# Kernel optimization log

Hardware: AMD Instinct MI355X
Metric: run time of the kernel (lower is better)

## Reference

```python
import jax, jax.numpy as jnp
import numpy as np

D_MODEL, D_INNER, D_STATE, D_CONV, DT_RANK = 2048, 4096, 16, 4, 128
B, T = 2, 1024


def setup_inputs() -> dict:
    key = jax.random.key(0)
    ks = jax.random.split(key, 8)
    dt_init_std = DT_RANK ** -0.5
    # dt bias init per the torch code: inv softplus of dt in [dt_min, dt_max]
    dt = jnp.exp(jax.random.uniform(ks[6], (D_INNER,)) * (np.log(0.1) - np.log(0.001)) + np.log(0.001))
    dt = jnp.clip(dt, 1e-4, None)
    dt_proj_b = dt + jnp.log(-jnp.expm1(-dt))
    A_log = jnp.log(jnp.tile(jnp.arange(1, D_STATE + 1, dtype=jnp.float32)[None, :], (D_INNER, 1)))
    return {
        "x": jax.random.normal(ks[0], (B, T, D_MODEL), jnp.float32),
        "h": jnp.zeros((B, D_INNER, D_STATE), jnp.float32),
        "conv_cache": jnp.zeros((B, D_INNER, D_CONV - 1), jnp.float32),
        "in_proj_w": jax.random.normal(ks[1], (2 * D_INNER, D_MODEL), jnp.float32) * 0.02,
        "conv_w": jax.random.normal(ks[2], (D_INNER, D_CONV), jnp.float32) * (1.0 / np.sqrt(D_CONV)),
        "conv_b": jnp.zeros((D_INNER,), jnp.float32),
        "x_proj_w": jax.random.normal(ks[3], (DT_RANK + 2 * D_STATE, D_INNER), jnp.float32) * 0.02,
        "dt_proj_w": jax.random.uniform(ks[4], (D_INNER, DT_RANK), jnp.float32, -dt_init_std, dt_init_std),
        "dt_proj_b": dt_proj_b,
        "A_log": A_log,
        "D_param": jnp.ones((D_INNER,), jnp.float32),
        "out_proj_w": jax.random.normal(ks[5], (D_MODEL, D_INNER), jnp.float32) * 0.02,
    }


def _forward(x, h, conv_cache, in_proj_w, conv_w, conv_b, x_proj_w,
             dt_proj_w, dt_proj_b, A_log, D_param, out_proj_w):
    Tlen = x.shape[1]
    xz = x @ in_proj_w.T                                  # (B,T,2*d_inner)
    xi, z = jnp.split(xz, 2, axis=-1)
    # causal depthwise conv with cache: concat history then valid conv
    xc = jnp.concatenate([jnp.swapaxes(conv_cache, 1, 2), xi], axis=1)  # (B,T+3,d_inner)
    new_conv_cache = jnp.swapaxes(xc[:, -(D_CONV - 1):, :], 1, 2)       # (B,d_inner,3)
    xconv = sum(xc[:, k:k + Tlen, :] * conv_w[:, k] for k in range(D_CONV)) + conv_b
    xs = jax.nn.silu(xconv)                               # (B,T,d_inner)
    # SSM params per step
    dbc = xs @ x_proj_w.T                                 # (B,T,dt_rank+2n)
    delta, Bm, Cm = jnp.split(dbc, [DT_RANK, DT_RANK + D_STATE], axis=-1)
    delta = jax.nn.softplus(delta @ dt_proj_w.T + dt_proj_b)  # (B,T,d_inner)
    A = -jnp.exp(A_log)                                   # (d_inner,n)
    dA = jnp.exp(jnp.einsum('btd,dn->btdn', delta, A))    # (B,T,d,n)
    dBx = jnp.einsum('btd,btn,btd->btdn', delta, Bm, xs)  # (B,T,d,n)

    def step(hc, inp):
        dA_t, dBx_t, C_t = inp
        hc = dA_t * hc + dBx_t                            # (B,d,n)
        return hc, jnp.einsum('bdn,bn->bd', hc, C_t)

    h_last, ys = jax.lax.scan(
        step, h,
        (jnp.moveaxis(dA, 1, 0), jnp.moveaxis(dBx, 1, 0), jnp.moveaxis(Cm, 1, 0)))
    y = jnp.moveaxis(ys, 0, 1) + D_param * xs             # (B,T,d_inner)
    out = (y * jax.nn.silu(z)) @ out_proj_w.T             # (B,T,d_model)
    return out, h_last, new_conv_cache


def reference(x, h, conv_cache, in_proj_w, conv_w, conv_b, x_proj_w,
              dt_proj_w, dt_proj_b, A_log, D_param, out_proj_w):
    return _forward(x, h, conv_cache, in_proj_w, conv_w, conv_b, x_proj_w,
                    dt_proj_w, dt_proj_b, A_log, D_param, out_proj_w)
```

## Files before the change

kernel.cpp:

```cpp
#include <hip/hip_runtime.h>
#include <hip/hip_bf16.h>
#include <math.h>

#define D_MODEL 2048
#define D_INNER 4096
#define D_STATE 16
#define D_CONV  4
#define DT_RANK 128
#define NB      2
#define TT      1024
#define M_TOT   (NB * TT)
#define NC      16
#define CL      64
#define TC      16

typedef __bf16 bf16x8_t __attribute__((ext_vector_type(8)));
typedef __bf16 bf16x4_t __attribute__((ext_vector_type(4)));
typedef float  f32x4_t  __attribute__((ext_vector_type(4)));

__global__ __launch_bounds__(256) void fused_cast(
    const float* __restrict__ x,  const float* __restrict__ wi,
    const float* __restrict__ wo, const float* __restrict__ wx,
    const float* __restrict__ wdt,
    __bf16* __restrict__ x16,  __bf16* __restrict__ wi16,
    __bf16* __restrict__ wo16, __bf16* __restrict__ wx16,
    __bf16* __restrict__ wdt16, __bf16* __restrict__ dbc16)
{
    const size_t g = (size_t)blockIdx.x * 256 + threadIdx.x;
    const float* src; __bf16* dst; size_t off;
    if      (g < 524288)  { src = x;   dst = x16;   off = g; }
    else if (g < 2621440) { src = wi;  dst = wi16;  off = g - 524288; }
    else if (g < 3670016) { src = wo;  dst = wo16;  off = g - 2621440; }
    else if (g < 3801088) { off = g - 3670016; dst = wx16;
                            src = (g < 3751936) ? wx : nullptr; }
    else if (g < 3866624) { src = wdt; dst = wdt16; off = g - 3801088; }
    else                  { src = nullptr; dst = dbc16; off = g - 3866624; }

    bf16x8_t v;
    if (src) {
        const float4 f0 = ((const float4*)src)[2 * off];
        const float4 f1 = ((const float4*)src)[2 * off + 1];
        v[0] = (__bf16)f0.x; v[1] = (__bf16)f0.y; v[2] = (__bf16)f0.z; v[3] = (__bf16)f0.w;
        v[4] = (__bf16)f1.x; v[5] = (__bf16)f1.y; v[6] = (__bf16)f1.z; v[7] = (__bf16)f1.w;
    } else {
        v = (bf16x8_t)(__bf16)0.f;
    }
    ((bf16x8_t*)dst)[off] = v;
}

__global__ __launch_bounds__(256) void reduce_out(
    const float4* __restrict__ p0, const float4* __restrict__ p1,
    float4* __restrict__ o)
{
    const size_t g = (size_t)blockIdx.x * 256 + threadIdx.x;
    const float4 a = p0[g];
    const float4 b = p1[g];
    o[g] = make_float4(a.x + b.x, a.y + b.y, a.z + b.z, a.w + b.w);
}

__global__ __launch_bounds__(512, 2) void gemm_bf16_256(
    const __bf16* __restrict__ A, int lda,
    const __bf16* __restrict__ W, int ldw,
    __bf16* __restrict__ C, int ldc,
    int nt)
{
    __shared__ __bf16 As[4 * 128 * 64];
    __shared__ __bf16 Bs[4 * 128 * 64];

    const int tid = threadIdx.x;
    const int w   = tid >> 6;
    const int l   = tid & 63;
    const int m0  = blockIdx.y * 256;
    const int n0  = blockIdx.x * 256;
    const int wm  = (w >> 2) * 128;
    const int wn  = (w & 3) * 64;

    const int sl   = ((l & 7) ^ (l >> 3)) & 7;
    const int srow = 2 * (w * 16 + (l >> 3)) + (sl >> 2);
    const int scol = (sl & 3) * 8;
    const __bf16* gA = A + (size_t)(m0 + srow) * lda + scol;
    const __bf16* gB = W + (size_t)(n0 + srow) * ldw + scol;
    __bf16* lA = &As[(size_t)w * 1024];
    __bf16* lB = &Bs[(size_t)w * 1024];

    const int fr  = l & 15;
    const int swz = ((((fr & 1) * 4) + (l >> 4)) ^ ((fr >> 1) & 7)) * 8;
    const int aoff = wm * 32 + (fr >> 1) * 64 + swz;
    const int boff = wn * 32 + (fr >> 1) * 64 + swz;

    f32x4_t acc[8][4] = {};

#define STAGE_A(t, q) { \
    const __bf16* s0_ = gA + (size_t)(t) * 32; \
    __builtin_amdgcn_global_load_lds((const __attribute__((address_space(1))) void*)s0_, \
        (__attribute__((address_space(3))) void*)(lA + (q) * 8192), 16, 0, 0); \
    __builtin_amdgcn_global_load_lds((const __attribute__((address_space(1))) void*)(s0_ + (size_t)16 * lda), \
        (__attribute__((address_space(3))) void*)(lA + (q) * 8192 + 512), 16, 0, 0); }
#define STAGE_B(t, q) { \
    const __bf16* s0_ = gB + (size_t)(t) * 32; \
    __builtin_amdgcn_global_load_lds((const __attribute__((address_space(1))) void*)s0_, \
        (__attribute__((address_space(3))) void*)(lB + (q) * 8192), 16, 0, 0); \
    __builtin_amdgcn_global_load_lds((const __attribute__((address_space(1))) void*)(s0_ + (size_t)16 * ldw), \
        (__attribute__((address_space(3))) void*)(lB + (q) * 8192 + 512), 16, 0, 0); }

    STAGE_A(0, 0); STAGE_B(0, 0);
    STAGE_A(1, 1); STAGE_B(1, 1);
    asm volatile("s_waitcnt vmcnt(4)" ::: "memory");
    __builtin_amdgcn_s_barrier();

    for (int t = 0; t < nt; ++t) {
        const int q  = t & 3;
        const int qn = (t + 2) & 3;
        const __bf16* Aq = &As[q * 8192];
        const __bf16* Bq = &Bs[q * 8192];
        bf16x8_t av[4], bv[4];

#pragma unroll
        for (int i = 0; i < 4; i++)
            av[i] = *(const bf16x8_t*)&Aq[aoff + i * 512];
#pragma unroll
        for (int i = 0; i < 4; i++)
            bv[i] = *(const bf16x8_t*)&Bq[boff + i * 512];
        if (t + 2 < nt) STAGE_A(t + 2, qn);
        __builtin_amdgcn_s_barrier();
        asm volatile("s_waitcnt lgkmcnt(0)" ::: "memory");
        __builtin_amdgcn_sched_barrier(0);
        __builtin_amdgcn_s_setprio(1);
#pragma unroll
        for (int mt = 0; mt < 4; mt++)
#pragma unroll
            for (int nn = 0; nn < 4; nn++)
                acc[mt][nn] = __builtin_amdgcn_mfma_f32_16x16x32_bf16(
                    av[mt], bv[nn], acc[mt][nn], 0, 0, 0);
        __builtin_amdgcn_s_setprio(0);
        __builtin_amdgcn_s_barrier();

#pragma unroll
        for (int i = 0; i < 4; i++)
            av[i] = *(const bf16x8_t*)&Aq[aoff + (i + 4) * 512];
        if (t + 2 < nt) STAGE_B(t + 2, qn);
        __builtin_amdgcn_s_barrier();
        asm volatile("s_waitcnt lgkmcnt(0)" ::: "memory");
        __builtin_amdgcn_sched_barrier(0);
        __builtin_amdgcn_s_setprio(1);
#pragma unroll
        for (int mt = 0; mt < 4; mt++)
#pragma unroll
            for (int nn = 0; nn < 4; nn++)
                acc[mt + 4][nn] = __builtin_amdgcn_mfma_f32_16x16x32_bf16(
                    av[mt], bv[nn], acc[mt + 4][nn], 0, 0, 0);
        __builtin_amdgcn_s_setprio(0);
        if (t + 2 < nt) asm volatile("s_waitcnt vmcnt(4)" ::: "memory");
        else            asm volatile("s_waitcnt vmcnt(0)" ::: "memory");
        __builtin_amdgcn_s_barrier();
    }
#undef STAGE_A
#undef STAGE_B

    const int cn = n0 + wn + fr;
    const int rb = m0 + wm + (l >> 4) * 4;
#pragma unroll
    for (int mt = 0; mt < 8; mt++)
#pragma unroll
        for (int nn = 0; nn < 4; nn++)
#pragma unroll
            for (int r = 0; r < 4; r++)
                C[(size_t)(rb + mt * 16 + r) * ldc + cn + nn * 16] =
                    (__bf16)acc[mt][nn][r];
}

template <int EPI, int KSTEP, typename OutT>
__global__ __launch_bounds__(256) void gemm_bf16_nt(
    const __bf16* __restrict__ A, int lda,
    const __bf16* __restrict__ W, int ldw,
    OutT* __restrict__ C, int ldc,
    int Kloop, int Nmax, const float* __restrict__ bias, size_t czoff)
{
    __shared__ __bf16 As[128 * KSTEP];
    __shared__ __bf16 Bs[128 * KSTEP];

    const int tid  = threadIdx.x;
    const int wave = tid >> 6;
    const int lane = tid & 63;
    const int m0 = blockIdx.y * 128;
    const int n0 = blockIdx.x * 128;
    const int mw = (wave >> 1) * 64;
    const int nw = (wave & 1) * 64;
    const int koff = blockIdx.z * Kloop;
    C += (size_t)blockIdx.z * czoff;

    f32x4_t acc[4][4] = {};

    const int g0 = wave * 2;
    const int rA = g0 * 16 + (lane >> 2);
    const int kk = (lane & 3) * 8;

    const __bf16* gA0 = A + (size_t)(m0 + rA) * lda + kk + koff;
    const __bf16* gA1 = gA0 + (size_t)16 * lda;
    const __bf16* gB0 = W + (size_t)(n0 + rA) * ldw + kk + koff;
    const __bf16* gB1 = gB0 + (size_t)16 * ldw;

    __bf16* lA0 = &As[(size_t)g0 * 512];
    __bf16* lA1 = &As[(size_t)(g0 + 1) * 512];
    __bf16* lB0 = &Bs[(size_t)g0 * 512];
    __bf16* lB1 = &Bs[(size_t)(g0 + 1) * 512];

    const int fr = lane & 15;
    const int fk = (lane >> 4) * 8;

    for (int k0 = 0; k0 < Kloop; k0 += KSTEP) {
#pragma unroll
        for (int p = 0; p < KSTEP / 32; p++) {
            const int kp = k0 + p * 32;
            const int lp = p * 4096;
            __builtin_amdgcn_global_load_lds(
                (const __attribute__((address_space(1))) void*)(gA0 + kp),
                (__attribute__((address_space(3))) void*)(lA0 + lp), 16, 0, 0);
            __builtin_amdgcn_global_load_lds(
                (const __attribute__((address_space(1))) void*)(gA1 + kp),
                (__attribute__((address_space(3))) void*)(lA1 + lp), 16, 0, 0);
            __builtin_amdgcn_global_load_lds(
                (const __attribute__((address_space(1))) void*)(gB0 + kp),
                (__attribute__((address_space(3))) void*)(lB0 + lp), 16, 0, 0);
            __builtin_amdgcn_global_load_lds(
                (const __attribute__((address_space(1))) void*)(gB1 + kp),
                (__attribute__((address_space(3))) void*)(lB1 + lp), 16, 0, 0);
        }
        __syncthreads();

#pragma unroll
        for (int p = 0; p < KSTEP / 32; p++) {
            const int lp = p * 4096;
            bf16x8_t av[4], bv[4];
#pragma unroll
            for (int mt = 0; mt < 4; mt++)
                av[mt] = *(const bf16x8_t*)&As[lp + (mw + mt * 16 + fr) * 32 + fk];
#pragma unroll
            for (int nt = 0; nt < 4; nt++)
                bv[nt] = *(const bf16x8_t*)&Bs[lp + (nw + nt * 16 + fr) * 32 + fk];

#pragma unroll
            for (int mt = 0; mt < 4; mt++)
#pragma unroll
                for (int nt = 0; nt < 4; nt++)
                    acc[mt][nt] = __builtin_amdgcn_mfma_f32_16x16x32_bf16(
                        av[mt], bv[nt], acc[mt][nt], 0, 0, 0);
        }
        __syncthreads();
    }

    const int cn = n0 + nw + (lane & 15);
    const int rb = m0 + mw + (lane >> 4) * 4;
#pragma unroll
    for (int mt = 0; mt < 4; mt++)
#pragma unroll
        for (int nt = 0; nt < 4; nt++) {
            const int n = cn + nt * 16;
            if (n >= Nmax) continue;
#pragma unroll
            for (int r = 0; r < 4; r++) {
                float v = acc[mt][nt][r];
                OutT* p = &C[(size_t)(rb + mt * 16 + r) * ldc + n];
                if (EPI == 1) {
                    v += bias[n];
                    v = (v > 20.f) ? v : __logf(1.f + __expf(v));
                    *p = (OutT)v;
                } else if (EPI == 2) {
                    atomicAdd((float*)p, v);
                } else {
                    *p = (OutT)v;
                }
            }
        }
}

__global__ __launch_bounds__(256) void gemm_dt(
    const float* __restrict__ A,
    const __bf16* __restrict__ W,
    __bf16* __restrict__ C,
    const float* __restrict__ bias)
{
    __shared__ __bf16 As[4 * 64 * 32];
    __shared__ __bf16 Bs[4 * 64 * 32];

    const int tid  = threadIdx.x;
    const int wave = tid >> 6;
    const int lane = tid & 63;
    const int m0 = blockIdx.y * 64;
    const int n0 = blockIdx.x * 64;
    const int mw = (wave >> 1) * 32;
    const int nw = (wave & 1) * 32;

    {
        const int r  = tid >> 2;
        const int cg = (tid & 3) * 8;
        const float* gA = A + (size_t)(m0 + r) * 160 + cg;
#pragma unroll
        for (int p = 0; p < 4; p++) {
            const float4 f0 = *(const float4*)(gA + p * 32);
            const float4 f1 = *(const float4*)(gA + p * 32 + 4);
            bf16x8_t v;
            v[0] = (__bf16)f0.x; v[1] = (__bf16)f0.y; v[2] = (__bf16)f0.z; v[3] = (__bf16)f0.w;
            v[4] = (__bf16)f1.x; v[5] = (__bf16)f1.y; v[6] = (__bf16)f1.z; v[7] = (__bf16)f1.w;
            *(bf16x8_t*)&As[p * 2048 + r * 32 + cg] = v;
        }
    }
    {
        const int rB = wave * 16 + (lane >> 2);
        const int kk = (lane & 3) * 8;
        const __bf16* gB = W + (size_t)(n0 + rB) * 128 + kk;
        __bf16* lB = &Bs[wave * 512];
#pragma unroll
        for (int p = 0; p < 4; p++) {
            __builtin_amdgcn_global_load_lds(
                (const __attribute__((address_space(1))) void*)(gB + p * 32),
                (__attribute__((address_space(3))) void*)(lB + p * 2048), 16, 0, 0);
        }
    }
    __syncthreads();

    const int fr = lane & 15;
    const int fk = (lane >> 4) * 8;
    f32x4_t acc[2][2] = {};
#pragma unroll
    for (int p = 0; p < 4; p++) {
        bf16x8_t av[2], bv[2];
#pragma unroll
        for (int mt = 0; mt < 2; mt++)
            av[mt] = *(const bf16x8_t*)&As[p * 2048 + (mw + mt * 16 + fr) * 32 + fk];
#pragma unroll
        for (int nt = 0; nt < 2; nt++)
            bv[nt] = *(const bf16x8_t*)&Bs[p * 2048 + (nw + nt * 16 + fr) * 32 + fk];
#pragma unroll
        for (int mt = 0; mt < 2; mt++)
#pragma unroll
            for (int nt = 0; nt < 2; nt++)
                acc[mt][nt] = __builtin_amdgcn_mfma_f32_16x16x32_bf16(
                    av[mt], bv[nt], acc[mt][nt], 0, 0, 0);
    }

    const int cn = n0 + nw + (lane & 15);
    const int rb = m0 + mw + (lane >> 4) * 4;
#pragma unroll
    for (int mt = 0; mt < 2; mt++)
#pragma unroll
        for (int nt = 0; nt < 2; nt++) {
            const int n = cn + nt * 16;
            const float bs = bias[n];
            bf16x4_t pk;
#pragma unroll
            for (int r = 0; r < 4; r++) {
                float v = acc[mt][nt][r] + bs;
                v = (v > 20.f) ? v : __logf(1.f + __expf(v));
                pk[r] = (__bf16)v;
            }
            const int m  = rb + mt * 16;
            const int bb = m >> 10;
            const int tt = m & 1023;
            *(bf16x4_t*)&C[((size_t)(bb * 4096 + n)) * 1024 + tt] = pk;
        }
}

__global__ __launch_bounds__(256) void conv_silu(
    const __bf16* __restrict__ xz16,
    const float* __restrict__ conv_cache,
    const float* __restrict__ conv_w,
    const float* __restrict__ conv_b,
    __bf16* __restrict__ xs16,
    __bf16* __restrict__ xsT,
    __bf16* __restrict__ zT,
    float* __restrict__ cc_out)
{
    __shared__ __bf16 Lxs[64][72];
    __shared__ __bf16 Lz[64][72];

    const int b  = blockIdx.z;
    const int D0 = blockIdx.y * 64;
    const int T0 = blockIdx.x * 64;
    const int dl = threadIdx.x & 63;
    const int tc = threadIdx.x >> 6;
    const int d  = D0 + dl;
    const int t0 = T0 + tc * TC;

    const float4 w  = *(const float4*)&conv_w[d * 4];
    const float bias = conv_b[d];

    float v[TC + 3];
    if (t0 == 0) {
        v[0] = conv_cache[(b * D_INNER + d) * 3 + 0];
        v[1] = conv_cache[(b * D_INNER + d) * 3 + 1];
        v[2] = conv_cache[(b * D_INNER + d) * 3 + 2];
    } else {
        v[0] = (float)xz16[(size_t)(b * TT + t0 - 3) * 8192 + d];
        v[1] = (float)xz16[(size_t)(b * TT + t0 - 2) * 8192 + d];
        v[2] = (float)xz16[(size_t)(b * TT + t0 - 1) * 8192 + d];
    }
#pragma unroll
    for (int k = 0; k < TC; k++)
        v[k + 3] = (float)xz16[(size_t)(b * TT + t0 + k) * 8192 + d];

#pragma unroll
    for (int k = 0; k < TC; k++) {
        float c = v[k] * w.x + v[k + 1] * w.y + v[k + 2] * w.z + v[k + 3] * w.w + bias;
        float s = c / (1.f + __expf(-c));
        xs16[(size_t)(b * TT + t0 + k) * 4096 + d] = (__bf16)s;
        Lxs[dl][tc * TC + k] = (__bf16)s;
    }
#pragma unroll
    for (int k = 0; k < TC; k++)
        Lz[dl][tc * TC + k] = xz16[(size_t)(b * TT + t0 + k) * 8192 + 4096 + d];

    if (t0 + TC == TT) {
        cc_out[(b * D_INNER + d) * 3 + 0] = v[TC];
        cc_out[(b * D_INNER + d) * 3 + 1] = v[TC + 1];
        cc_out[(b * D_INNER + d) * 3 + 2] = v[TC + 2];
    }

    __syncthreads();

    const int d2 = threadIdx.x >> 2;
    const int tq = (threadIdx.x & 3) * 16;
    const size_t to = ((size_t)(b * 4096 + D0 + d2)) * 1024 + T0 + tq;
    *(bf16x8_t*)&xsT[to]     = *(const bf16x8_t*)&Lxs[d2][tq];
    *(bf16x8_t*)&xsT[to + 8] = *(const bf16x8_t*)&Lxs[d2][tq + 8];
    *(bf16x8_t*)&zT[to]      = *(const bf16x8_t*)&Lz[d2][tq];
    *(bf16x8_t*)&zT[to + 8]  = *(const bf16x8_t*)&Lz[d2][tq + 8];
}

__global__ __launch_bounds__(256) void scan_phase_a(
    const __bf16* __restrict__ deltaT,
    const float* __restrict__ dbc,
    const __bf16* __restrict__ xsT,
    const float* __restrict__ A_log,
    float* __restrict__ P,
    float* __restrict__ S)
{
    const int idx = blockIdx.x * 256 + threadIdx.x;
    const int sub = idx & 3;
    const int d   = (idx >> 2) & 4095;
    const int c   = (idx >> 14) & (NC - 1);
    const int b   = idx >> 18;

    const float4 Af = *(const float4*)&A_log[d * 16 + sub * 4];
    const float Ad0 = -__expf(Af.x), Ad1 = -__expf(Af.y);
    const float Ad2 = -__expf(Af.z), Ad3 = -__expf(Af.w);

    const size_t tb = ((size_t)(b * 4096 + d)) * 1024 + c * CL;
    const __bf16* pdT = deltaT + tb;
    const __bf16* pxT = xsT + tb;
    const float*  pB  = dbc + ((size_t)b * TT + c * CL) * 160 + 128 + sub * 4;

    float h0 = 0.f, h1 = 0.f, h2 = 0.f, h3 = 0.f, sd = 0.f;
    for (int to = 0; to < CL; to += 8) {
        const bf16x8_t dv = *(const bf16x8_t*)&pdT[to];
        const bf16x8_t xv = *(const bf16x8_t*)&pxT[to];
#pragma unroll
        for (int k = 0; k < 8; k++) {
            const float delta = (float)dv[k];
            const float x     = (float)xv[k];
            const float4 Bv   = *(const float4*)&pB[(size_t)(to + k) * 160];
            const float dx = delta * x;
            h0 = __expf(delta * Ad0) * h0 + dx * Bv.x;
            h1 = __expf(delta * Ad1) * h1 + dx * Bv.y;
            h2 = __expf(delta * Ad2) * h2 + dx * Bv.z;
            h3 = __expf(delta * Ad3) * h3 + dx * Bv.w;
            sd += delta;
        }
    }
    const size_t o = ((size_t)(b * NC + c) * 4096 + d) * 16 + sub * 4;
    *(float4*)&P[o] = make_float4(__expf(Ad0 * sd), __expf(Ad1 * sd),
                                  __expf(Ad2 * sd), __expf(Ad3 * sd));
    *(float4*)&S[o] = make_float4(h0, h1, h2, h3);
}

__global__ __launch_bounds__(256) void scan_phase_c(
    const __bf16* __restrict__ deltaT,
    const __bf16* __restrict__ zT,
    const float* __restrict__ dbc,
    const __bf16* __restrict__ xsT,
    const float* __restrict__ P,
    const float* __restrict__ S,
    const float* __restrict__ h_in,
    const float* __restrict__ A_log,
    const float* __restrict__ D_param,
    __bf16* __restrict__ ys16,
    float* __restrict__ h_out)
{
    const int idx = blockIdx.x * 256 + threadIdx.x;
    const int sub = idx & 3;
    const int d   = (idx >> 2) & 4095;
    const int c   = (idx >> 14) & (NC - 1);
    const int b   = idx >> 18;

    const float4 Af = *(const float4*)&A_log[d * 16 + sub * 4];
    const float Ad0 = -__expf(Af.x), Ad1 = -__expf(Af.y);
    const float Ad2 = -__expf(Af.z), Ad3 = -__expf(Af.w);
    const float Dp = D_param[d];

    float4 hf = *(const float4*)&h_in[((size_t)b * 4096 + d) * 16 + sub * 4];
    float h0 = hf.x, h1 = hf.y, h2 = hf.z, h3 = hf.w;
    for (int cc = 0; cc < c; cc++) {
        const size_t o2 = ((size_t)(b * NC + cc) * 4096 + d) * 16 + sub * 4;
        const float4 p = *(const float4*)&P[o2];
        const float4 s = *(const float4*)&S[o2];
        h0 = p.x * h0 + s.x;
        h1 = p.y * h1 + s.y;
        h2 = p.z * h2 + s.z;
        h3 = p.w * h3 + s.w;
    }

    const size_t tb = ((size_t)(b * 4096 + d)) * 1024 + c * CL;
    const __bf16* pdT = deltaT + tb;
    const __bf16* pxT = xsT + tb;
    const __bf16* pzT = zT + tb;
    const float*  pB  = dbc + ((size_t)b * TT + c * CL) * 160 + 128 + sub * 4;
    const float*  pC  = pB + 16;
    __bf16* py = ys16 + ((size_t)b * TT + c * CL) * 4096 + d;

    for (int to = 0; to < CL; to += 8) {
        const bf16x8_t dv  = *(const bf16x8_t*)&pdT[to];
        const bf16x8_t xv8 = *(const bf16x8_t*)&pxT[to];
        const bf16x8_t zv8 = *(const bf16x8_t*)&pzT[to];
#pragma unroll
        for (int k = 0; k < 8; k++) {
            const float delta = (float)dv[k];
            const float x     = (float)xv8[k];
            const float4 Bv   = *(const float4*)&pB[(size_t)(to + k) * 160];
            const float4 Cv   = *(const float4*)&pC[(size_t)(to + k) * 160];
            const float dx = delta * x;

            h0 = __expf(delta * Ad0) * h0 + dx * Bv.x;
            h1 = __expf(delta * Ad1) * h1 + dx * Bv.y;
            h2 = __expf(delta * Ad2) * h2 + dx * Bv.z;
            h3 = __expf(delta * Ad3) * h3 + dx * Bv.w;

            float y = h0 * Cv.x + h1 * Cv.y + h2 * Cv.z + h3 * Cv.w;
            y += __shfl_xor(y, 1);
            y += __shfl_xor(y, 2);

            if (sub == 0) {
                const float zv = (float)zv8[k];
                y += Dp * x;
                const float g = zv / (1.f + __expf(-zv));
                py[(size_t)(to + k) * 4096] = (__bf16)(y * g);
            }
        }
    }

    if (c == NC - 1) {
        *(float4*)&h_out[((size_t)b * 4096 + d) * 16 + sub * 4] =
            make_float4(h0, h1, h2, h3);
    }
}

extern "C" void kernel_launch(void* const* d_in, const int* in_sizes, int n_in,
                              void* d_out, int out_size, void* d_ws, size_t ws_size,
                              hipStream_t stream)
{
    const float* x          = (const float*)d_in[0];
    const float* h_in       = (const float*)d_in[1];
    const float* conv_cache = (const float*)d_in[2];
    const float* in_proj_w  = (const float*)d_in[3];
    const float* conv_w     = (const float*)d_in[4];
    const float* conv_b     = (const float*)d_in[5];
    const float* x_proj_w   = (const float*)d_in[6];
    const float* dt_proj_w  = (const float*)d_in[7];
    const float* dt_proj_b  = (const float*)d_in[8];
    const float* A_log      = (const float*)d_in[9];
    const float* D_param    = (const float*)d_in[10];
    const float* out_proj_w = (const float*)d_in[11];

    float* out    = (float*)d_out;
    float* h_out  = (float*)d_out + (size_t)NB * TT * D_MODEL;
    float* cc_out = h_out + (size_t)NB * D_INNER * D_STATE;

    char* ws = (char*)d_ws;
    __bf16* xz16    = (__bf16*)(ws);
    float*  Pbuf    = (float*)(ws);
    float*  Sbuf    = (float*)(ws + 8388608);
    float*  Pout    = (float*)(ws);
    __bf16* wi16    = (__bf16*)(ws + 33554432);
    __bf16* xsT     = (__bf16*)(ws + 33554432);
    __bf16* zT      = (__bf16*)(ws + 50331648);
    __bf16* x16     = (__bf16*)(ws + 67108864);
    __bf16* deltaT  = (__bf16*)(ws + 67108864);
    __bf16* wo16    = (__bf16*)(ws + 83886080);
    __bf16* xs16    = (__bf16*)(ws + 100663296);
    __bf16* ys16    = (__bf16*)(ws + 100663296);
    __bf16* wx16    = (__bf16*)(ws + 117440512);
    __bf16* wdt16   = (__bf16*)(ws + 119537664);
    float*  dbc     = (float*)(ws + 120586240);

    dim3 blk(256);

    fused_cast<<<dim3(15424), blk, 0, stream>>>(
        x, in_proj_w, out_proj_w, x_proj_w, dt_proj_w,
        x16, wi16, wo16, wx16, wdt16, (__bf16*)dbc);

    gemm_bf16_256<<<dim3(32, 8), dim3(512), 0, stream>>>(
        x16, 2048, wi16, 2048, xz16, 8192, 2048 / 32);

    conv_silu<<<dim3(TT / 64, D_INNER / 64, NB), blk, 0, stream>>>(
        xz16, conv_cache, conv_w, conv_b, xs16, xsT, zT, cc_out);

    gemm_bf16_nt<2, 64, float><<<dim3(2, 16, 16), blk, 0, stream>>>(
        xs16, 4096, wx16, 4096, dbc, 160, 256, 160, nullptr, 0);

    gemm_dt<<<dim3(64, 32), blk, 0, stream>>>(dbc, wdt16, deltaT, dt_proj_b);

    scan_phase_a<<<dim3(NB * D_INNER * NC * 4 / 256), blk, 0, stream>>>(
        deltaT, dbc, xsT, A_log, Pbuf, Sbuf);
    scan_phase_c<<<dim3(NB * D_INNER * NC * 4 / 256), blk, 0, stream>>>(
        deltaT, zT, dbc, xsT, Pbuf, Sbuf, h_in, A_log, D_param, ys16, h_out);

    gemm_bf16_nt<0, 64, float><<<dim3(16, 16, 2), blk, 0, stream>>>(
        ys16, 4096, wo16, 4096, Pout, 2048, 2048, 2048, nullptr,
        (size_t)2048 * 2048);
    reduce_out<<<dim3(4096), blk, 0, stream>>>(
        (const float4*)Pout, (const float4*)(Pout + (size_t)2048 * 2048),
        (float4*)out);
}
```

Before: 429.8 us.

## Software-pipeline LDS fragment reads in 256 GEMM and reuse it for out_proj split-K

Restructures the 256x256 GEMM main loop so the next K-step's A/B fragment reads from LDS are issued before the current MFMAs, with partial lgkmcnt waits, overlapping LDS latency with compute. The loop is unrolled by two with ping-pong register sets. The kernel also gains split-K over blockIdx.z and a templated output type, so the output projection now uses this GEMM with 4-way split-K and a 4-input reduction instead of the 128-tile GEMM with 2-way split. This raises register pressure, and the 4-way split adds partial-sum traffic in exchange for a better tile and more blocks.

```diff
diff --git a/kernel.cpp b/kernel.cpp
--- a/kernel.cpp
+++ b/kernel.cpp
@@ -48,21 +48,26 @@
     ((bf16x8_t*)dst)[off] = v;
 }
 
-__global__ __launch_bounds__(256) void reduce_out(
+__global__ __launch_bounds__(256) void reduce_out4(
     const float4* __restrict__ p0, const float4* __restrict__ p1,
+    const float4* __restrict__ p2, const float4* __restrict__ p3,
     float4* __restrict__ o)
 {
     const size_t g = (size_t)blockIdx.x * 256 + threadIdx.x;
     const float4 a = p0[g];
     const float4 b = p1[g];
-    o[g] = make_float4(a.x + b.x, a.y + b.y, a.z + b.z, a.w + b.w);
-}
-
+    const float4 c = p2[g];
+    const float4 d = p3[g];
+    o[g] = make_float4(a.x + b.x + c.x + d.x, a.y + b.y + c.y + d.y,
+                       a.z + b.z + c.z + d.z, a.w + b.w + c.w + d.w);
+}
+
+template <typename OutT>
 __global__ __launch_bounds__(512, 2) void gemm_bf16_256(
     const __bf16* __restrict__ A, int lda,
     const __bf16* __restrict__ W, int ldw,
-    __bf16* __restrict__ C, int ldc,
-    int nt)
+    OutT* __restrict__ C, int ldc,
+    int nt, size_t czoff)
 {
     __shared__ __bf16 As[4 * 128 * 64];
     __shared__ __bf16 Bs[4 * 128 * 64];
@@ -74,12 +79,14 @@
     const int n0  = blockIdx.x * 256;
     const int wm  = (w >> 2) * 128;
     const int wn  = (w & 3) * 64;
+    const int koff = blockIdx.z * nt * 32;
+    C += (size_t)blockIdx.z * czoff;
 
     const int sl   = ((l & 7) ^ (l >> 3)) & 7;
     const int srow = 2 * (w * 16 + (l >> 3)) + (sl >> 2);
     const int scol = (sl & 3) * 8;
-    const __bf16* gA = A + (size_t)(m0 + srow) * lda + scol;
-    const __bf16* gB = W + (size_t)(n0 + srow) * ldw + scol;
+    const __bf16* gA = A + (size_t)(m0 + srow) * lda + scol + koff;
+    const __bf16* gB = W + (size_t)(n0 + srow) * ldw + scol + koff;
     __bf16* lA = &As[(size_t)w * 1024];
     __bf16* lB = &Bs[(size_t)w * 1024];
 
@@ -89,6 +96,7 @@
     const int boff = wn * 32 + (fr >> 1) * 64 + swz;
 
     f32x4_t acc[8][4] = {};
+    bf16x8_t aL[4], aH[4], b0[4], aLn[4], b0n[4];
 
 #define STAGE_A(t, q) { \
     const __bf16* s0_ = gA + (size_t)(t) * 32; \
@@ -107,53 +115,65 @@
     STAGE_A(1, 1); STAGE_B(1, 1);
     asm volatile("s_waitcnt vmcnt(4)" ::: "memory");
     __builtin_amdgcn_s_barrier();
-
-    for (int t = 0; t < nt; ++t) {
-        const int q  = t & 3;
-        const int qn = (t + 2) & 3;
-        const __bf16* Aq = &As[q * 8192];
-        const __bf16* Bq = &Bs[q * 8192];
-        bf16x8_t av[4], bv[4];
-
-#pragma unroll
-        for (int i = 0; i < 4; i++)
-            av[i] = *(const bf16x8_t*)&Aq[aoff + i * 512];
-#pragma unroll
-        for (int i = 0; i < 4; i++)
-            bv[i] = *(const bf16x8_t*)&Bq[boff + i * 512];
-        if (t + 2 < nt) STAGE_A(t + 2, qn);
-        __builtin_amdgcn_s_barrier();
-        asm volatile("s_waitcnt lgkmcnt(0)" ::: "memory");
-        __builtin_amdgcn_sched_barrier(0);
-        __builtin_amdgcn_s_setprio(1);
-#pragma unroll
-        for (int mt = 0; mt < 4; mt++)
-#pragma unroll
-            for (int nn = 0; nn < 4; nn++)
-                acc[mt][nn] = __builtin_amdgcn_mfma_f32_16x16x32_bf16(
-                    av[mt], bv[nn], acc[mt][nn], 0, 0, 0);
-        __builtin_amdgcn_s_setprio(0);
-        __builtin_amdgcn_s_barrier();
-
-#pragma unroll
-        for (int i = 0; i < 4; i++)
-            av[i] = *(const bf16x8_t*)&Aq[aoff + (i + 4) * 512];
-        if (t + 2 < nt) STAGE_B(t + 2, qn);
-        __builtin_amdgcn_s_barrier();
-        asm volatile("s_waitcnt lgkmcnt(0)" ::: "memory");
-        __builtin_amdgcn_sched_barrier(0);
-        __builtin_amdgcn_s_setprio(1);
-#pragma unroll
-        for (int mt = 0; mt < 4; mt++)
-#pragma unroll
-            for (int nn = 0; nn < 4; nn++)
-                acc[mt + 4][nn] = __builtin_amdgcn_mfma_f32_16x16x32_bf16(
-                    av[mt], bv[nn], acc[mt + 4][nn], 0, 0, 0);
-        __builtin_amdgcn_s_setprio(0);
-        if (t + 2 < nt) asm volatile("s_waitcnt vmcnt(4)" ::: "memory");
-        else            asm volatile("s_waitcnt vmcnt(0)" ::: "memory");
-        __builtin_amdgcn_s_barrier();
-    }
+#pragma unroll
+    for (int i = 0; i < 4; i++) aL[i] = *(const bf16x8_t*)&As[aoff + i * 512];
+#pragma unroll
+    for (int i = 0; i < 4; i++) b0[i] = *(const bf16x8_t*)&Bs[boff + i * 512];
+
+#define PH0(t, CL_, CB_) { \
+    const __bf16* Aq_ = &As[((t) & 3) * 8192]; \
+    _Pragma("unroll") \
+    for (int i = 0; i < 4; i++) \
+        aH[i] = *(const bf16x8_t*)&Aq_[aoff + (i + 4) * 512]; \
+    if ((t) + 2 < nt) STAGE_A((t) + 2, ((t) + 2) & 3); \
+    __builtin_amdgcn_s_barrier(); \
+    asm volatile("s_waitcnt lgkmcnt(4)" ::: "memory"); \
+    __builtin_amdgcn_sched_barrier(0); \
+    __builtin_amdgcn_s_setprio(1); \
+    _Pragma("unroll") \
+    for (int mt = 0; mt < 4; mt++) \
+        _Pragma("unroll") \
+        for (int nn = 0; nn < 4; nn++) \
+            acc[mt][nn] = __builtin_amdgcn_mfma_f32_16x16x32_bf16( \
+                CL_[mt], CB_[nn], acc[mt][nn], 0, 0, 0); \
+    __builtin_amdgcn_s_setprio(0); \
+    if ((t) + 2 < nt) asm volatile("s_waitcnt vmcnt(2)" ::: "memory"); \
+    else              asm volatile("s_waitcnt vmcnt(0)" ::: "memory"); \
+    __builtin_amdgcn_s_barrier(); }
+
+#define PH1(t, CB_, NL_, NB_) { \
+    const __bf16* An_ = &As[(((t) + 1) & 3) * 8192]; \
+    const __bf16* Bn_ = &Bs[(((t) + 1) & 3) * 8192]; \
+    const bool rd_ = (t) + 1 < nt; \
+    if (rd_) { \
+        _Pragma("unroll") \
+        for (int i = 0; i < 4; i++) NL_[i] = *(const bf16x8_t*)&An_[aoff + i * 512]; \
+        _Pragma("unroll") \
+        for (int i = 0; i < 4; i++) NB_[i] = *(const bf16x8_t*)&Bn_[boff + i * 512]; \
+    } \
+    if ((t) + 2 < nt) STAGE_B((t) + 2, ((t) + 2) & 3); \
+    __builtin_amdgcn_s_barrier(); \
+    if (rd_) asm volatile("s_waitcnt lgkmcnt(8)" ::: "memory"); \
+    else     asm volatile("s_waitcnt lgkmcnt(0)" ::: "memory"); \
+    __builtin_amdgcn_sched_barrier(0); \
+    __builtin_amdgcn_s_setprio(1); \
+    _Pragma("unroll") \
+    for (int mt = 0; mt < 4; mt++) \
+        _Pragma("unroll") \
+        for (int nn = 0; nn < 4; nn++) \
+            acc[mt + 4][nn] = __builtin_amdgcn_mfma_f32_16x16x32_bf16( \
+                aH[mt], CB_[nn], acc[mt + 4][nn], 0, 0, 0); \
+    __builtin_amdgcn_s_setprio(0); \
+    __builtin_amdgcn_s_barrier(); }
+
+    for (int t = 0; t < nt; t += 2) {
+        PH0(t, aL, b0);
+        PH1(t, b0, aLn, b0n);
+        PH0(t + 1, aLn, b0n);
+        PH1(t + 1, b0n, aL, b0);
+    }
+#undef PH0
+#undef PH1
 #undef STAGE_A
 #undef STAGE_B
 
@@ -166,7 +186,7 @@
 #pragma unroll
             for (int r = 0; r < 4; r++)
                 C[(size_t)(rb + mt * 16 + r) * ldc + cn + nn * 16] =
-                    (__bf16)acc[mt][nn][r];
+                    (OutT)acc[mt][nn][r];
 }
 
 template <int EPI, int KSTEP, typename OutT>
@@ -592,13 +612,14 @@
     float*  dbc     = (float*)(ws + 120586240);
 
     dim3 blk(256);
+    const size_t NOUT = (size_t)2048 * 2048;
 
     fused_cast<<<dim3(15424), blk, 0, stream>>>(
         x, in_proj_w, out_proj_w, x_proj_w, dt_proj_w,
         x16, wi16, wo16, wx16, wdt16, (__bf16*)dbc);
 
-    gemm_bf16_256<<<dim3(32, 8), dim3(512), 0, stream>>>(
-        x16, 2048, wi16, 2048, xz16, 8192, 2048 / 32);
+    gemm_bf16_256<__bf16><<<dim3(32, 8, 1), dim3(512), 0, stream>>>(
+        x16, 2048, wi16, 2048, xz16, 8192, 2048 / 32, 0);
 
     conv_silu<<<dim3(TT / 64, D_INNER / 64, NB), blk, 0, stream>>>(
         xz16, conv_cache, conv_w, conv_b, xs16, xsT, zT, cc_out);
@@ -613,10 +634,10 @@
     scan_phase_c<<<dim3(NB * D_INNER * NC * 4 / 256), blk, 0, stream>>>(
         deltaT, zT, dbc, xsT, Pbuf, Sbuf, h_in, A_log, D_param, ys16, h_out);
 
-    gemm_bf16_nt<0, 64, float><<<dim3(16, 16, 2), blk, 0, stream>>>(
-        ys16, 4096, wo16, 4096, Pout, 2048, 2048, 2048, nullptr,
-        (size_t)2048 * 2048);
-    reduce_out<<<dim3(4096), blk, 0, stream>>>(
-        (const float4*)Pout, (const float4*)(Pout + (size_t)2048 * 2048),
+    gemm_bf16_256<float><<<dim3(8, 8, 4), dim3(512), 0, stream>>>(
+        ys16, 4096, wo16, 4096, Pout, 2048, 1024 / 32, NOUT);
+    reduce_out4<<<dim3(4096), blk, 0, stream>>>(
+        (const float4*)Pout, (const float4*)(Pout + NOUT),
+        (const float4*)(Pout + 2 * NOUT), (const float4*)(Pout + 3 * NOUT),
         (float4*)out);
 }
```

After: 437.6 us. No clear change (+1.8%).

## Shrink in_proj GEMM tile to 128x256 with triple-buffered single-phase pipeline

Applied to the files above, without the earlier changes.

Replaces the 256x256 in_proj GEMM tile with a 128x256 tile, which doubles the grid to 512 blocks. The tile is triple-buffered, with one staging call and one barrier per K-step instead of a two-phase ping-pong split. Each block now uses less LDS and fewer accumulators, which should allow higher occupancy and better spread across CUs. In exchange, B-tile reuse per block drops, so weights are reloaded twice as often. There are also fewer independent MFMAs per barrier to hide load latency.

```diff
diff --git a/kernel.cpp b/kernel.cpp
--- a/kernel.cpp
+++ b/kernel.cpp
@@ -58,29 +58,30 @@
     o[g] = make_float4(a.x + b.x, a.y + b.y, a.z + b.z, a.w + b.w);
 }
 
-__global__ __launch_bounds__(512, 2) void gemm_bf16_256(
+__global__ __launch_bounds__(512, 4) void gemm_in128(
     const __bf16* __restrict__ A, int lda,
     const __bf16* __restrict__ W, int ldw,
     __bf16* __restrict__ C, int ldc,
     int nt)
 {
-    __shared__ __bf16 As[4 * 128 * 64];
-    __shared__ __bf16 Bs[4 * 128 * 64];
+    __shared__ __bf16 As[3 * 4096];
+    __shared__ __bf16 Bs[3 * 8192];
 
     const int tid = threadIdx.x;
     const int w   = tid >> 6;
     const int l   = tid & 63;
-    const int m0  = blockIdx.y * 256;
+    const int m0  = blockIdx.y * 128;
     const int n0  = blockIdx.x * 256;
-    const int wm  = (w >> 2) * 128;
+    const int wm  = (w >> 2) * 64;
     const int wn  = (w & 3) * 64;
 
-    const int sl   = ((l & 7) ^ (l >> 3)) & 7;
-    const int srow = 2 * (w * 16 + (l >> 3)) + (sl >> 2);
+    const int sl  = ((l & 7) ^ (l >> 3)) & 7;
+    const int srA = 2 * (w * 8  + (l >> 3)) + (sl >> 2);
+    const int srB = 2 * (w * 16 + (l >> 3)) + (sl >> 2);
     const int scol = (sl & 3) * 8;
-    const __bf16* gA = A + (size_t)(m0 + srow) * lda + scol;
-    const __bf16* gB = W + (size_t)(n0 + srow) * ldw + scol;
-    __bf16* lA = &As[(size_t)w * 1024];
+    const __bf16* gA = A + (size_t)(m0 + srA) * lda + scol;
+    const __bf16* gB = W + (size_t)(n0 + srB) * ldw + scol;
+    __bf16* lA = &As[(size_t)w * 512];
     __bf16* lB = &Bs[(size_t)w * 1024];
 
     const int fr  = l & 15;
@@ -88,41 +89,35 @@
     const int aoff = wm * 32 + (fr >> 1) * 64 + swz;
     const int boff = wn * 32 + (fr >> 1) * 64 + swz;
 
-    f32x4_t acc[8][4] = {};
-
-#define STAGE_A(t, q) { \
-    const __bf16* s0_ = gA + (size_t)(t) * 32; \
-    __builtin_amdgcn_global_load_lds((const __attribute__((address_space(1))) void*)s0_, \
-        (__attribute__((address_space(3))) void*)(lA + (q) * 8192), 16, 0, 0); \
-    __builtin_amdgcn_global_load_lds((const __attribute__((address_space(1))) void*)(s0_ + (size_t)16 * lda), \
-        (__attribute__((address_space(3))) void*)(lA + (q) * 8192 + 512), 16, 0, 0); }
-#define STAGE_B(t, q) { \
-    const __bf16* s0_ = gB + (size_t)(t) * 32; \
-    __builtin_amdgcn_global_load_lds((const __attribute__((address_space(1))) void*)s0_, \
+    f32x4_t acc[4][4] = {};
+
+#define STAGE(t, q) { \
+    const __bf16* a_ = gA + (size_t)(t) * 32; \
+    const __bf16* b_ = gB + (size_t)(t) * 32; \
+    __builtin_amdgcn_global_load_lds((const __attribute__((address_space(1))) void*)a_, \
+        (__attribute__((address_space(3))) void*)(lA + (q) * 4096), 16, 0, 0); \
+    __builtin_amdgcn_global_load_lds((const __attribute__((address_space(1))) void*)b_, \
         (__attribute__((address_space(3))) void*)(lB + (q) * 8192), 16, 0, 0); \
-    __builtin_amdgcn_global_load_lds((const __attribute__((address_space(1))) void*)(s0_ + (size_t)16 * ldw), \
+    __builtin_amdgcn_global_load_lds((const __attribute__((address_space(1))) void*)(b_ + (size_t)16 * ldw), \
         (__attribute__((address_space(3))) void*)(lB + (q) * 8192 + 512), 16, 0, 0); }
 
-    STAGE_A(0, 0); STAGE_B(0, 0);
-    STAGE_A(1, 1); STAGE_B(1, 1);
-    asm volatile("s_waitcnt vmcnt(4)" ::: "memory");
+    STAGE(0, 0);
+    STAGE(1, 1);
+    asm volatile("s_waitcnt vmcnt(3)" ::: "memory");
     __builtin_amdgcn_s_barrier();
 
     for (int t = 0; t < nt; ++t) {
-        const int q  = t & 3;
-        const int qn = (t + 2) & 3;
-        const __bf16* Aq = &As[q * 8192];
+        const int q = t % 3;
+        if (t + 2 < nt) STAGE(t + 2, (t + 2) % 3);
+        const __bf16* Aq = &As[q * 4096];
         const __bf16* Bq = &Bs[q * 8192];
         bf16x8_t av[4], bv[4];
-
 #pragma unroll
         for (int i = 0; i < 4; i++)
             av[i] = *(const bf16x8_t*)&Aq[aoff + i * 512];
 #pragma unroll
         for (int i = 0; i < 4; i++)
             bv[i] = *(const bf16x8_t*)&Bq[boff + i * 512];
-        if (t + 2 < nt) STAGE_A(t + 2, qn);
-        __builtin_amdgcn_s_barrier();
         asm volatile("s_waitcnt lgkmcnt(0)" ::: "memory");
         __builtin_amdgcn_sched_barrier(0);
         __builtin_amdgcn_s_setprio(1);
@@ -133,34 +128,16 @@
                 acc[mt][nn] = __builtin_amdgcn_mfma_f32_16x16x32_bf16(
                     av[mt], bv[nn], acc[mt][nn], 0, 0, 0);
         __builtin_amdgcn_s_setprio(0);
-        __builtin_amdgcn_s_barrier();
-
-#pragma unroll
-        for (int i = 0; i < 4; i++)
-            av[i] = *(const bf16x8_t*)&Aq[aoff + (i + 4) * 512];
-        if (t + 2 < nt) STAGE_B(t + 2, qn);
-        __builtin_amdgcn_s_barrier();
-        asm volatile("s_waitcnt lgkmcnt(0)" ::: "memory");
-        __builtin_amdgcn_sched_barrier(0);
-        __builtin_amdgcn_s_setprio(1);
-#pragma unroll
-        for (int mt = 0; mt < 4; mt++)
-#pragma unroll
-            for (int nn = 0; nn < 4; nn++)
-                acc[mt + 4][nn] = __builtin_amdgcn_mfma_f32_16x16x32_bf16(
-                    av[mt], bv[nn], acc[mt + 4][nn], 0, 0, 0);
-        __builtin_amdgcn_s_setprio(0);
-        if (t + 2 < nt) asm volatile("s_waitcnt vmcnt(4)" ::: "memory");
+        if (t + 2 < nt) asm volatile("s_waitcnt vmcnt(3)" ::: "memory");
         else            asm volatile("s_waitcnt vmcnt(0)" ::: "memory");
         __builtin_amdgcn_s_barrier();
     }
-#undef STAGE_A
-#undef STAGE_B
+#undef STAGE
 
     const int cn = n0 + wn + fr;
     const int rb = m0 + wm + (l >> 4) * 4;
 #pragma unroll
-    for (int mt = 0; mt < 8; mt++)
+    for (int mt = 0; mt < 4; mt++)
 #pragma unroll
         for (int nn = 0; nn < 4; nn++)
 #pragma unroll
@@ -592,12 +569,13 @@
     float*  dbc     = (float*)(ws + 120586240);
 
     dim3 blk(256);
+    const size_t NOUT = (size_t)2048 * 2048;
 
     fused_cast<<<dim3(15424), blk, 0, stream>>>(
         x, in_proj_w, out_proj_w, x_proj_w, dt_proj_w,
         x16, wi16, wo16, wx16, wdt16, (__bf16*)dbc);
 
-    gemm_bf16_256<<<dim3(32, 8), dim3(512), 0, stream>>>(
+    gemm_in128<<<dim3(32, 16), dim3(512), 0, stream>>>(
         x16, 2048, wi16, 2048, xz16, 8192, 2048 / 32);
 
     conv_silu<<<dim3(TT / 64, D_INNER / 64, NB), blk, 0, stream>>>(
@@ -614,9 +592,7 @@
         deltaT, zT, dbc, xsT, Pbuf, Sbuf, h_in, A_log, D_param, ys16, h_out);
 
     gemm_bf16_nt<0, 64, float><<<dim3(16, 16, 2), blk, 0, stream>>>(
-        ys16, 4096, wo16, 4096, Pout, 2048, 2048, 2048, nullptr,
-        (size_t)2048 * 2048);
+        ys16, 4096, wo16, 4096, Pout, 2048, 2048, 2048, nullptr, NOUT);
     reduce_out<<<dim3(4096), blk, 0, stream>>>(
-        (const float4*)Pout, (const float4*)(Pout + (size_t)2048 * 2048),
-        (float4*)out);
-}
+        (const float4*)Pout, (const float4*)(Pout + NOUT), (float4*)out);
+}
```

Measured after the change: 434.6 us. Within noise of the previous version (+1.1%).
